# Optimization experiments

Hardware: AMD Instinct MI355X
Metric: run time of the kernel (lower is better)

Reference implementation:

```python
import jax, jax.numpy as jnp
import numpy as np

NUM_HEADS = 32
NUM_KV_HEADS = 8
HEAD_DIM = 128  # hidden_size 4096 / 32 heads
ROPE_BASE = 10000.0


def setup_inputs() -> dict:
    key = jax.random.key(0)
    ks = jax.random.split(key, 5)
    H = NUM_HEADS * HEAD_DIM
    KV = NUM_KV_HEADS * HEAD_DIM
    B, S = 1, 2048
    s = 0.02
    return {
        "hidden_states": jax.random.normal(ks[0], (B, S, H), dtype=jnp.float32),
        "Wq": jax.random.normal(ks[1], (H, H), dtype=jnp.float32) * s,
        "Wk": jax.random.normal(ks[2], (H, KV), dtype=jnp.float32) * s,
        "Wv": jax.random.normal(ks[3], (H, KV), dtype=jnp.float32) * s,
        "Wo": jax.random.normal(ks[4], (H, H), dtype=jnp.float32) * s,
    }


def _rope_tables(seq_len, head_dim, dtype):
    inv_freq = 1.0 / (ROPE_BASE ** (jnp.arange(0, head_dim, 2, dtype=jnp.float32) / head_dim))
    freqs = jnp.arange(seq_len, dtype=jnp.float32)[:, None] * inv_freq[None, :]  # [S, hd/2]
    emb = jnp.concatenate([freqs, freqs], axis=-1)  # [S, hd]
    return emb.astype(dtype)  # angles; cos/sin taken by caller


def _rotate_half(x):
    x1, x2 = jnp.split(x, 2, axis=-1)
    return jnp.concatenate([-x2, x1], axis=-1)


def reference(hidden_states, Wq, Wk, Wv, Wo):
    B, S, H = hidden_states.shape
    hd = HEAD_DIM
    scale = hd ** -0.5

    q = (hidden_states @ Wq).reshape(B, S, NUM_HEADS, hd).transpose(0, 2, 1, 3)      # [B,nh,S,hd]
    k = (hidden_states @ Wk).reshape(B, S, NUM_KV_HEADS, hd).transpose(0, 2, 1, 3)   # [B,nkv,S,hd]
    v = (hidden_states @ Wv).reshape(B, S, NUM_KV_HEADS, hd).transpose(0, 2, 1, 3)

    ang = _rope_tables(S, hd, hidden_states.dtype)          # [S, hd]
    cos = jnp.cos(ang)[None, None]                          # [1,1,S,hd]
    sin = jnp.sin(ang)[None, None]
    q = q * cos + _rotate_half(q) * sin
    k = k * cos + _rotate_half(k) * sin

    rep = NUM_HEADS // NUM_KV_HEADS
    if rep > 1:
        k = jnp.repeat(k, rep, axis=1)  # matches torch repeat_interleave on head dim
        v = jnp.repeat(v, rep, axis=1)

    scores = jnp.einsum("bhqd,bhkd->bhqk", q, k) * scale    # [B,nh,S,S]
    causal = jnp.triu(jnp.ones((S, S), dtype=bool), k=1)
    scores = jnp.where(causal[None, None], jnp.float32(-jnp.inf).astype(scores.dtype), scores)
    weights = jax.nn.softmax(scores, axis=-1)
    attn = jnp.einsum("bhqk,bhkd->bhqd", weights, v)        # [B,nh,S,hd]
    out = attn.transpose(0, 2, 1, 3).reshape(B, S, H) @ Wo  # [B,S,H]
    return (out, k, v)
```

## Files before the change

kernel.cpp:

```cpp
#include <hip/hip_runtime.h>
#include <hip/hip_bf16.h>
#include <math.h>

typedef __bf16 bf16_t;
typedef bf16_t bf16x8 __attribute__((ext_vector_type(8)));
typedef bf16_t bf16x4 __attribute__((ext_vector_type(4)));
typedef float  f32x4  __attribute__((ext_vector_type(4)));

#define AS1(p) ((__attribute__((address_space(1))) void*)(p))
#define AS3(p) ((__attribute__((address_space(3))) void*)(p))

__global__ void convert_f32_bf16(const float* __restrict__ in, bf16_t* __restrict__ out)
{
    int i = blockIdx.x * 256 + threadIdx.x;
    float4 v = ((const float4*)in)[i];
    bf16x4 o;
    o[0] = (bf16_t)v.x; o[1] = (bf16_t)v.y; o[2] = (bf16_t)v.z; o[3] = (bf16_t)v.w;
    ((bf16x4*)out)[i] = o;
}

__global__ void transpose_convert(const float* __restrict__ W, bf16_t* __restrict__ Wt,
                                  int K, int N)
{
    __shared__ float tile[32][33];
    const int n0 = blockIdx.x * 32;
    const int k0 = blockIdx.y * 32;
    const int r = threadIdx.x >> 5;
    const int c = threadIdx.x & 31;
    #pragma unroll
    for (int i = 0; i < 32; i += 8)
        tile[r + i][c] = W[(size_t)(k0 + r + i) * N + n0 + c];
    __syncthreads();
    #pragma unroll
    for (int i = 0; i < 32; i += 8)
        Wt[(size_t)(n0 + r + i) * K + k0 + c] = (bf16_t)tile[c][r + i];
}

template <typename OutT>
__global__ __launch_bounds__(256)
void gemm_bt_128(const bf16_t* __restrict__ A, const bf16_t* __restrict__ Bt,
                 OutT* __restrict__ C, int M, int N, int K)
{
    __shared__ bf16_t As[128 * 32];
    __shared__ bf16_t Bs[128 * 32];
    const int t    = threadIdx.x;
    const int lane = t & 63;
    const int wave = t >> 6;

    const int nwg   = gridDim.x * gridDim.y;
    int bid = blockIdx.x + blockIdx.y * gridDim.x;
    const int chunk = nwg >> 3;
    bid = (bid & 7) * chunk + (bid >> 3);
    const int m0 = (bid % gridDim.x) * 128;
    const int n0 = (bid / gridDim.x) * 128;

    const int wm = (wave & 1) * 64;
    const int wn = (wave >> 1) * 64;
    const int lm = lane & 15;
    const int lq = lane >> 4;

    f32x4 acc[4][4] = {};

    const int chunk0 = wave * 64 + lane;
    const int r0 = chunk0 >> 2, c0 = (chunk0 & 3) * 8;
    const int chunk1 = 256 + chunk0;
    const int r1 = chunk1 >> 2, c1 = (chunk1 & 3) * 8;

    const bf16_t* Ag0 = A  + (size_t)(m0 + r0) * K + c0;
    const bf16_t* Ag1 = A  + (size_t)(m0 + r1) * K + c1;
    const bf16_t* Bg0 = Bt + (size_t)(n0 + r0) * K + c0;
    const bf16_t* Bg1 = Bt + (size_t)(n0 + r1) * K + c1;
    bf16_t* As0 = As + (wave * 64) * 8;
    bf16_t* As1 = As + (256 + wave * 64) * 8;
    bf16_t* Bs0 = Bs + (wave * 64) * 8;
    bf16_t* Bs1 = Bs + (256 + wave * 64) * 8;

    for (int k0 = 0; k0 < K; k0 += 32) {
        __syncthreads();
        __builtin_amdgcn_global_load_lds(AS1(Ag0 + k0), AS3(As0), 16, 0, 0);
        __builtin_amdgcn_global_load_lds(AS1(Ag1 + k0), AS3(As1), 16, 0, 0);
        __builtin_amdgcn_global_load_lds(AS1(Bg0 + k0), AS3(Bs0), 16, 0, 0);
        __builtin_amdgcn_global_load_lds(AS1(Bg1 + k0), AS3(Bs1), 16, 0, 0);
        __syncthreads();

        bf16x8 af[4], bb[4];
        #pragma unroll
        for (int mt = 0; mt < 4; ++mt)
            af[mt] = *(const bf16x8*)(As + (wm + mt * 16 + lm) * 32 + lq * 8);
        #pragma unroll
        for (int nt = 0; nt < 4; ++nt)
            bb[nt] = *(const bf16x8*)(Bs + (wn + nt * 16 + lm) * 32 + lq * 8);
        #pragma unroll
        for (int mt = 0; mt < 4; ++mt)
            #pragma unroll
            for (int nt = 0; nt < 4; ++nt)
                acc[mt][nt] = __builtin_amdgcn_mfma_f32_16x16x32_bf16(
                    af[mt], bb[nt], acc[mt][nt], 0, 0, 0);
    }

    #pragma unroll
    for (int mt = 0; mt < 4; ++mt) {
        #pragma unroll
        for (int nt = 0; nt < 4; ++nt) {
            const int row = m0 + wm + mt * 16 + lq * 4;
            const int col = n0 + wn + nt * 16 + lm;
            #pragma unroll
            for (int r = 0; r < 4; ++r) {
                float v = acc[mt][nt][r];
                if constexpr (sizeof(OutT) == 2)
                    C[(size_t)(row + r) * N + col] = (OutT)(bf16_t)v;
                else
                    C[(size_t)(row + r) * N + col] = v;
            }
        }
    }
}

__global__ void rope_qk(bf16_t* __restrict__ QKV, float* __restrict__ k_out, int S)
{
    int idx  = blockIdx.x * 256 + threadIdx.x;
    int d    = idx & 63;
    int s    = idx >> 6;
    int head = blockIdx.y;
    float ang = (float)s * exp2f((float)d * -0.20762050593f);
    float sn, cs;
    sincosf(ang, &sn, &cs);
    int col = head < 32 ? head * 128 : 4096 + (head - 32) * 128;
    bf16_t* p = QKV + (size_t)s * 6144 + col;
    float x1 = (float)p[d], x2 = (float)p[d + 64];
    float y1 = x1 * cs - x2 * sn;
    float y2 = x2 * cs + x1 * sn;
    p[d]      = (bf16_t)y1;
    p[d + 64] = (bf16_t)y2;
    if (head >= 32) {
        int g = head - 32;
        #pragma unroll
        for (int j = 0; j < 4; ++j) {
            float* kb = k_out + ((size_t)(g * 4 + j) * S + s) * 128;
            kb[d]      = y1;
            kb[d + 64] = y2;
        }
    }
}

__global__ void v_finish(const bf16_t* __restrict__ QKV, float* __restrict__ v_out,
                         bf16_t* __restrict__ Vt, int S)
{
    __shared__ bf16_t tl[32][33];
    const int s0  = blockIdx.x * 32;
    const int gd0 = blockIdx.y * 32;
    const int r = threadIdx.x >> 5;
    const int c = threadIdx.x & 31;
    #pragma unroll
    for (int i = 0; i < 32; i += 8) {
        int s = s0 + r + i;
        bf16_t v = QKV[(size_t)s * 6144 + 5120 + gd0 + c];
        tl[r + i][c] = v;
        int gd = gd0 + c;
        int g = gd >> 7, d = gd & 127;
        float vf = (float)v;
        #pragma unroll
        for (int j = 0; j < 4; ++j)
            v_out[((size_t)(g * 4 + j) * S + s) * 128 + d] = vf;
    }
    __syncthreads();
    #pragma unroll
    for (int i = 0; i < 32; i += 8)
        Vt[(size_t)(gd0 + r + i) * S + s0 + c] = tl[c][r + i];
}

__global__ void pack_frags(const bf16_t* __restrict__ QKV, const bf16_t* __restrict__ Vt,
                           bf16_t* __restrict__ Kfrag, bf16_t* __restrict__ Vfrag, int S)
{
    const int b  = blockIdx.x;
    const int g  = b >> 5, kt = b & 31;
    const int t  = threadIdx.x;
    bf16x8* Kf = (bf16x8*)Kfrag + (size_t)b * 1024;
    bf16x8* Vf = (bf16x8*)Vfrag + (size_t)b * 1024;
    #pragma unroll
    for (int i = 0; i < 4; ++i) {
        int slot = i * 256 + t;
        int f = slot >> 6, l = slot & 63;
        int kk = f >> 2, nt = f & 3, lm = l & 15, lq = l >> 4;
        Kf[slot] = *(const bf16x8*)(QKV + (size_t)(kt * 64 + nt * 16 + lm) * 6144
                                    + 4096 + g * 128 + kk * 32 + lq * 8);
    }
    #pragma unroll
    for (int i = 0; i < 4; ++i) {
        int slot = i * 256 + t;
        int f = slot >> 6, l = slot & 63;
        int kk = f >> 3, nt = f & 7, lm = l & 15, lq = l >> 4;
        Vf[slot] = *(const bf16x8*)(Vt + (size_t)(g * 128 + nt * 16 + lm) * S
                                    + kt * 64 + kk * 32 + lq * 8);
    }
}

__global__ __launch_bounds__(256, 2)
void attn_fwd(const bf16_t* __restrict__ QKV,
              const bf16_t* __restrict__ Kfrag, const bf16_t* __restrict__ Vfrag,
              bf16_t* __restrict__ O, int S)
{
    const int b    = blockIdx.x;
    const int g    = b & 7;
    const int idx  = b >> 3;
    const int h    = g * 4 + (idx & 3);
    const int c    = 63 - (idx >> 2);
    const int wave = threadIdx.x >> 6;
    const int lane = threadIdx.x & 63;
    const int lm   = lane & 15;
    const int lq   = lane >> 4;
    const int q0   = c * 32;

    __shared__ __align__(16) char smem[19456];
    bf16_t* P  = (bf16_t*)smem + wave * (32 * 72);
    float*  Cb = (float*)smem;
    float*  ml = (float*)(smem + 18432);

    bf16x8 aq[2][4];
    #pragma unroll
    for (int mi = 0; mi < 2; ++mi) {
        const bf16_t* qrow = QKV + (size_t)(q0 + mi * 16 + lm) * 6144 + h * 128;
        #pragma unroll
        for (int kk = 0; kk < 4; ++kk)
            aq[mi][kk] = *(const bf16x8*)(qrow + kk * 32 + lq * 8);
    }

    f32x4 acc[2][8] = {};
    float mrow[2][4], lrow[2][4];
    #pragma unroll
    for (int mi = 0; mi < 2; ++mi)
        #pragma unroll
        for (int r = 0; r < 4; ++r) { mrow[mi][r] = -3.0e38f; lrow[mi][r] = 0.f; }
    const float scale = 0.08838834764831845f;

    const int nkt = (q0 >> 6) + 1;

    for (int kt = wave; kt < nkt; kt += 4) {
        const int k0 = kt * 64;
        const bf16x8* Kf = (const bf16x8*)Kfrag + ((size_t)(g * 32 + kt) << 10);
        const bf16x8* Vf = (const bf16x8*)Vfrag + ((size_t)(g * 32 + kt) << 10);

        bf16x8 bk[4][4];
        #pragma unroll
        for (int kk = 0; kk < 4; ++kk)
            #pragma unroll
            for (int nt = 0; nt < 4; ++nt)
                bk[kk][nt] = Kf[(kk * 4 + nt) * 64 + lane];

        f32x4 sc[2][4] = {};
        #pragma unroll
        for (int kk = 0; kk < 4; ++kk)
            #pragma unroll
            for (int nt = 0; nt < 4; ++nt)
                #pragma unroll
                for (int mi = 0; mi < 2; ++mi)
                    sc[mi][nt] = __builtin_amdgcn_mfma_f32_16x16x32_bf16(
                        aq[mi][kk], bk[kk][nt], sc[mi][nt], 0, 0, 0);

        bf16x8 bv[2][8];
        #pragma unroll
        for (int kk = 0; kk < 2; ++kk)
            #pragma unroll
            for (int nt = 0; nt < 8; ++nt)
                bv[kk][nt] = Vf[(kk * 8 + nt) * 64 + lane];

        #pragma unroll
        for (int mi = 0; mi < 2; ++mi)
            #pragma unroll
            for (int nt = 0; nt < 4; ++nt)
                #pragma unroll
                for (int r = 0; r < 4; ++r)
                    sc[mi][nt][r] *= scale;

        if (kt == nkt - 1) {
            #pragma unroll
            for (int mi = 0; mi < 2; ++mi)
                #pragma unroll
                for (int nt = 0; nt < 4; ++nt) {
                    int col = k0 + nt * 16 + lm;
                    #pragma unroll
                    for (int r = 0; r < 4; ++r) {
                        int row = q0 + mi * 16 + lq * 4 + r;
                        if (col > row) sc[mi][nt][r] = -3.0e38f;
                    }
                }
        }

        #pragma unroll
        for (int mi = 0; mi < 2; ++mi) {
            float tmax[4];
            #pragma unroll
            for (int r = 0; r < 4; ++r)
                tmax[r] = fmaxf(fmaxf(sc[mi][0][r], sc[mi][1][r]),
                                fmaxf(sc[mi][2][r], sc[mi][3][r]));
            #pragma unroll
            for (int off = 1; off < 16; off <<= 1)
                #pragma unroll
                for (int r = 0; r < 4; ++r)
                    tmax[r] = fmaxf(tmax[r], __shfl_xor(tmax[r], off));

            float alpha[4];
            #pragma unroll
            for (int r = 0; r < 4; ++r) {
                float mn = fmaxf(mrow[mi][r], tmax[r]);
                alpha[r] = __expf(mrow[mi][r] - mn);
                mrow[mi][r] = mn;
            }
            float rsum[4] = {0.f, 0.f, 0.f, 0.f};
            #pragma unroll
            for (int nt = 0; nt < 4; ++nt)
                #pragma unroll
                for (int r = 0; r < 4; ++r) {
                    float p = __expf(sc[mi][nt][r] - mrow[mi][r]);
                    sc[mi][nt][r] = p;
                    rsum[r] += p;
                }
            #pragma unroll
            for (int off = 1; off < 16; off <<= 1)
                #pragma unroll
                for (int r = 0; r < 4; ++r)
                    rsum[r] += __shfl_xor(rsum[r], off);
            #pragma unroll
            for (int r = 0; r < 4; ++r)
                lrow[mi][r] = lrow[mi][r] * alpha[r] + rsum[r];
            #pragma unroll
            for (int nt = 0; nt < 8; ++nt)
                #pragma unroll
                for (int r = 0; r < 4; ++r)
                    acc[mi][nt][r] *= alpha[r];

            #pragma unroll
            for (int nt = 0; nt < 4; ++nt)
                #pragma unroll
                for (int r = 0; r < 4; ++r)
                    P[(mi * 16 + lq * 4 + r) * 72 + nt * 16 + lm] = (bf16_t)sc[mi][nt][r];
        }

        bf16x8 ap[2][2];
        #pragma unroll
        for (int mi = 0; mi < 2; ++mi)
            #pragma unroll
            for (int kk = 0; kk < 2; ++kk)
                ap[mi][kk] = *(const bf16x8*)(P + (mi * 16 + lm) * 72 + kk * 32 + lq * 8);

        #pragma unroll
        for (int kk = 0; kk < 2; ++kk)
            #pragma unroll
            for (int nt = 0; nt < 8; ++nt)
                #pragma unroll
                for (int mi = 0; mi < 2; ++mi)
                    acc[mi][nt] = __builtin_amdgcn_mfma_f32_16x16x32_bf16(
                        ap[mi][kk], bv[kk][nt], acc[mi][nt], 0, 0, 0);
    }

    if (lm == 0) {
        #pragma unroll
        for (int mi = 0; mi < 2; ++mi)
            #pragma unroll
            for (int r = 0; r < 4; ++r) {
                int lr = mi * 16 + lq * 4 + r;
                ml[(wave * 2 + 0) * 32 + lr] = mrow[mi][r];
                ml[(wave * 2 + 1) * 32 + lr] = lrow[mi][r];
            }
    }
    __syncthreads();

    float fac[2][4], linv[2][4];
    #pragma unroll
    for (int mi = 0; mi < 2; ++mi)
        #pragma unroll
        for (int r = 0; r < 4; ++r) {
            int lr = mi * 16 + lq * 4 + r;
            float m0 = ml[0 * 32 + lr], m1 = ml[2 * 32 + lr];
            float m2 = ml[4 * 32 + lr], m3 = ml[6 * 32 + lr];
            float mg = fmaxf(fmaxf(m0, m1), fmaxf(m2, m3));
            float ls = ml[1 * 32 + lr] * __expf(m0 - mg)
                     + ml[3 * 32 + lr] * __expf(m1 - mg)
                     + ml[5 * 32 + lr] * __expf(m2 - mg)
                     + ml[7 * 32 + lr] * __expf(m3 - mg);
            fac[mi][r]  = __expf(mrow[mi][r] - mg);
            linv[mi][r] = 1.0f / ls;
        }

    for (int w = 0; w < 3; ++w) {
        if (wave == w) {
            #pragma unroll
            for (int mi = 0; mi < 2; ++mi)
                #pragma unroll
                for (int nt = 0; nt < 8; ++nt)
                    #pragma unroll
                    for (int r = 0; r < 4; ++r) {
                        int lr = mi * 16 + lq * 4 + r;
                        int col = nt * 16 + lm;
                        float v = acc[mi][nt][r] * fac[mi][r];
                        if (w == 0) Cb[lr * 132 + col] = v;
                        else        Cb[lr * 132 + col] += v;
                    }
        }
        __syncthreads();
    }
    if (wave == 3) {
        #pragma unroll
        for (int mi = 0; mi < 2; ++mi)
            #pragma unroll
            for (int nt = 0; nt < 8; ++nt)
                #pragma unroll
                for (int r = 0; r < 4; ++r) {
                    int lr = mi * 16 + lq * 4 + r;
                    int col = nt * 16 + lm;
                    float v = Cb[lr * 132 + col] + acc[mi][nt][r] * fac[mi][r];
                    O[(size_t)(q0 + lr) * 4096 + h * 128 + col] =
                        (bf16_t)(v * linv[mi][r]);
                }
    }
}

extern "C" void kernel_launch(void* const* d_in, const int* in_sizes, int n_in,
                              void* d_out, int out_size, void* d_ws, size_t ws_size,
                              hipStream_t stream)
{
    const float* hidden = (const float*)d_in[0];
    const float* Wq = (const float*)d_in[1];
    const float* Wk = (const float*)d_in[2];
    const float* Wv = (const float*)d_in[3];
    const float* Wo = (const float*)d_in[4];

    const int S = 2048, H = 4096, KV = 1024, NQKV = 6144;

    char* ws = (char*)d_ws;
    bf16_t* hid_b  = (bf16_t*)(ws);
    bf16_t* Wqkv_t = (bf16_t*)(ws + (size_t)(16u  << 20));
    bf16_t* Wo_t   = (bf16_t*)(ws + (size_t)(64u  << 20));
    bf16_t* QKV    = (bf16_t*)(ws + (size_t)(96u  << 20));
    bf16_t* Vt     = (bf16_t*)(ws + (size_t)(120u << 20));
    bf16_t* attn   = (bf16_t*)(ws + (size_t)(124u << 20));
    bf16_t* Kfrag  = (bf16_t*)(ws);
    bf16_t* Vfrag  = (bf16_t*)(ws + (size_t)(4u << 20));

    float* out_o = (float*)d_out;
    float* out_k = out_o + (size_t)S * H;
    float* out_v = out_k + (size_t)32 * S * 128;

    convert_f32_bf16<<<S * H / 4 / 256, 256, 0, stream>>>(hidden, hid_b);
    transpose_convert<<<dim3(H / 32, H / 32), 256, 0, stream>>>(Wq, Wqkv_t, H, H);
    transpose_convert<<<dim3(KV / 32, H / 32), 256, 0, stream>>>(Wk, Wqkv_t + (size_t)4096 * H, H, KV);
    transpose_convert<<<dim3(KV / 32, H / 32), 256, 0, stream>>>(Wv, Wqkv_t + (size_t)5120 * H, H, KV);
    transpose_convert<<<dim3(H / 32, H / 32), 256, 0, stream>>>(Wo, Wo_t, H, H);

    gemm_bt_128<bf16_t><<<dim3(S / 128, NQKV / 128), 256, 0, stream>>>(hid_b, Wqkv_t, QKV, S, NQKV, H);

    rope_qk<<<dim3(S * 64 / 256, 40), 256, 0, stream>>>(QKV, out_k, S);
    v_finish<<<dim3(S / 32, KV / 32), 256, 0, stream>>>(QKV, out_v, Vt, S);
    pack_frags<<<256, 256, 0, stream>>>(QKV, Vt, Kfrag, Vfrag, S);

    attn_fwd<<<2048, 256, 0, stream>>>(QKV, Kfrag, Vfrag, attn, S);

    gemm_bt_128<float><<<dim3(S / 128, H / 128), 256, 0, stream>>>(attn, Wo_t, out_o, S, H, H);
}
```

Before: 596.0 us.

## Double GEMM K-tile to 64 with XOR-swizzled LDS layout

The bf16 GEMM now stages a 128x64 K-slice per iteration instead of 128x32, which halves the number of barrier pairs per output tile. Global-to-LDS loads use an XOR swizzle of the 16-byte column group by row, and the fragment reads apply the same swizzle to avoid LDS bank conflicts across the wider 128-byte rows. LDS use doubles to 32 KB per block, which could reduce occupancy, and there is still no double buffering.

```diff
diff --git a/kernel.cpp b/kernel.cpp
--- a/kernel.cpp
+++ b/kernel.cpp
@@ -41,8 +41,8 @@
 void gemm_bt_128(const bf16_t* __restrict__ A, const bf16_t* __restrict__ Bt,
                  OutT* __restrict__ C, int M, int N, int K)
 {
-    __shared__ bf16_t As[128 * 32];
-    __shared__ bf16_t Bs[128 * 32];
+    __shared__ bf16_t As[128 * 64];
+    __shared__ bf16_t Bs[128 * 64];
     const int t    = threadIdx.x;
     const int lane = t & 63;
     const int wave = t >> 6;
@@ -61,41 +61,42 @@
 
     f32x4 acc[4][4] = {};
 
-    const int chunk0 = wave * 64 + lane;
-    const int r0 = chunk0 >> 2, c0 = (chunk0 & 3) * 8;
-    const int chunk1 = 256 + chunk0;
-    const int r1 = chunk1 >> 2, c1 = (chunk1 & 3) * 8;
-
-    const bf16_t* Ag0 = A  + (size_t)(m0 + r0) * K + c0;
-    const bf16_t* Ag1 = A  + (size_t)(m0 + r1) * K + c1;
-    const bf16_t* Bg0 = Bt + (size_t)(n0 + r0) * K + c0;
-    const bf16_t* Bg1 = Bt + (size_t)(n0 + r1) * K + c1;
-    bf16_t* As0 = As + (wave * 64) * 8;
-    bf16_t* As1 = As + (256 + wave * 64) * 8;
-    bf16_t* Bs0 = Bs + (wave * 64) * 8;
-    bf16_t* Bs1 = Bs + (256 + wave * 64) * 8;
-
-    for (int k0 = 0; k0 < K; k0 += 32) {
+    const int sr = t >> 3;
+    const int sg = ((t & 7) ^ (sr & 7)) * 8;
+    const bf16_t* Ag = A  + (size_t)(m0 + sr) * K + sg;
+    const bf16_t* Bg = Bt + (size_t)(n0 + sr) * K + sg;
+    bf16_t* AsW = As + wave * 512;
+    bf16_t* BsW = Bs + wave * 512;
+
+    for (int k0 = 0; k0 < K; k0 += 64) {
         __syncthreads();
-        __builtin_amdgcn_global_load_lds(AS1(Ag0 + k0), AS3(As0), 16, 0, 0);
-        __builtin_amdgcn_global_load_lds(AS1(Ag1 + k0), AS3(As1), 16, 0, 0);
-        __builtin_amdgcn_global_load_lds(AS1(Bg0 + k0), AS3(Bs0), 16, 0, 0);
-        __builtin_amdgcn_global_load_lds(AS1(Bg1 + k0), AS3(Bs1), 16, 0, 0);
+        #pragma unroll
+        for (int i = 0; i < 4; ++i) {
+            __builtin_amdgcn_global_load_lds(AS1(Ag + (size_t)(i * 32) * K + k0),
+                                             AS3(AsW + i * 2048), 16, 0, 0);
+            __builtin_amdgcn_global_load_lds(AS1(Bg + (size_t)(i * 32) * K + k0),
+                                             AS3(BsW + i * 2048), 16, 0, 0);
+        }
         __syncthreads();
 
-        bf16x8 af[4], bb[4];
-        #pragma unroll
-        for (int mt = 0; mt < 4; ++mt)
-            af[mt] = *(const bf16x8*)(As + (wm + mt * 16 + lm) * 32 + lq * 8);
-        #pragma unroll
-        for (int nt = 0; nt < 4; ++nt)
-            bb[nt] = *(const bf16x8*)(Bs + (wn + nt * 16 + lm) * 32 + lq * 8);
-        #pragma unroll
-        for (int mt = 0; mt < 4; ++mt)
-            #pragma unroll
-            for (int nt = 0; nt < 4; ++nt)
-                acc[mt][nt] = __builtin_amdgcn_mfma_f32_16x16x32_bf16(
-                    af[mt], bb[nt], acc[mt][nt], 0, 0, 0);
+        #pragma unroll
+        for (int kk = 0; kk < 2; ++kk) {
+            bf16x8 af[4], bb[4];
+            #pragma unroll
+            for (int mt = 0; mt < 4; ++mt)
+                af[mt] = *(const bf16x8*)(As + (wm + mt * 16 + lm) * 64
+                                          + (((kk * 4 + lq) ^ (lm & 7)) * 8));
+            #pragma unroll
+            for (int nt = 0; nt < 4; ++nt)
+                bb[nt] = *(const bf16x8*)(Bs + (wn + nt * 16 + lm) * 64
+                                          + (((kk * 4 + lq) ^ (lm & 7)) * 8));
+            #pragma unroll
+            for (int mt = 0; mt < 4; ++mt)
+                #pragma unroll
+                for (int nt = 0; nt < 4; ++nt)
+                    acc[mt][nt] = __builtin_amdgcn_mfma_f32_16x16x32_bf16(
+                        af[mt], bb[nt], acc[mt][nt], 0, 0, 0);
+        }
     }
 
     #pragma unroll
```

Measured after the change: 562.5 us. 5.6% less time.
